# Kernel tuning notes

Measured on AMD Instinct MI355X. Metric: run time of the kernel, lower is better.

The kernel has to match this reference:

```python
import jax, jax.numpy as jnp
import numpy as np


def setup_inputs() -> dict:
    key = jax.random.key(0)
    ks = jax.random.split(key, 7)
    B, T, E, H, V = 32, 200, 32, 128, 8000
    s = lambda fan: 1.0 / np.sqrt(fan)
    return {
        "x": jax.random.normal(ks[0], (B, T, E), dtype=jnp.float32),
        "Ww": jax.random.normal(ks[1], (H, H), dtype=jnp.float32) * s(H),
        "Wb": jax.random.normal(ks[2], (H,), dtype=jnp.float32) * s(H),
        "Uw": jax.random.normal(ks[3], (H, E), dtype=jnp.float32) * s(E),
        "Ub": jax.random.normal(ks[4], (H,), dtype=jnp.float32) * s(E),
        "Vw": jax.random.normal(ks[5], (V, H), dtype=jnp.float32) * s(H),
        "Vb": jax.random.normal(ks[6], (V,), dtype=jnp.float32) * s(H),
    }


def reference(x, Ww, Wb, Uw, Ub, Vw, Vb):
    # x: [B, T, E]. Elman RNN: h_t = tanh(W h_{t-1} + b_W + U x_t + b_U); out_t = V h_t + b_V
    B = x.shape[0]
    H = Ww.shape[0]
    h0 = jnp.zeros((B, H), dtype=x.dtype)
    # Precompute input projections for all timesteps at once: [T, B, H]
    ux = jnp.einsum('bte,he->tbh', x, Uw) + Ub + Wb

    def step(h, ux_t):
        h = jnp.tanh(h @ Ww.T + ux_t)
        return h, h

    hidden, hs = jax.lax.scan(step, h0, ux)  # hs: [T, B, H]
    # Output projection applied to all hidden states (same math as per-step V)
    out_seq = jnp.einsum('tbh,vh->btv', hs, Vw) + Vb  # [B, T, V]
    return out_seq, hidden
```

## Files before the change

### kernel.cpp

```cpp
#include <hip/hip_runtime.h>
#include <stdint.h>

typedef short v8s __attribute__((ext_vector_type(8)));
typedef float v4f __attribute__((ext_vector_type(4)));

__device__ __forceinline__ float bf2f(short s) {
    unsigned int u = ((unsigned int)(unsigned short)s) << 16;
    float f; __builtin_memcpy(&f, &u, 4); return f;
}
__device__ __forceinline__ unsigned short f2bf_rne(float f) {
    unsigned int u; __builtin_memcpy(&u, &f, 4);
    return (unsigned short)((u + 0x7FFFu + ((u >> 16) & 1u)) >> 16);
}
__device__ __forceinline__ unsigned short f2bf_rhu(float f) {
    unsigned int u; __builtin_memcpy(&u, &f, 4);
    return (unsigned short)((u + 0x8000u) >> 16);
}
__device__ __forceinline__ unsigned short f2bf_trunc(float f) {
    unsigned int u; __builtin_memcpy(&u, &f, 4);
    return (unsigned short)(u >> 16);
}
__device__ __forceinline__ float tanh_fast(float z) {
    float e = __expf(2.0f * z);
    float r = __builtin_amdgcn_rcpf(e + 1.0f);
    return __builtin_fmaf(-2.0f, r, 1.0f);
}

__global__ __launch_bounds__(256) void ux_kernel(
    const float* __restrict__ x, const float* __restrict__ Uw,
    const float* __restrict__ Ub, const float* __restrict__ Wb,
    float* __restrict__ ux, unsigned* __restrict__ sync) {
    if (blockIdx.x == 0) {
        for (int i = threadIdx.x; i < 864; i += 256) sync[i] = 0;
    }
    int row = blockIdx.x * 2 + (threadIdx.x >> 7);
    int i = threadIdx.x & 127;
    int b = row & 31, t = row >> 5;
    const float* xr = x + (b * 200 + t) * 32;
    const float* ur = Uw + i * 32;
    float acc = 0.f;
#pragma unroll
    for (int e4 = 0; e4 < 8; ++e4) {
        v4f xv = *(const v4f*)(xr + e4 * 4);
        v4f uv = *(const v4f*)(ur + e4 * 4);
#pragma unroll
        for (int j = 0; j < 4; ++j) acc = __builtin_fmaf(xv[j], uv[j], acc);
    }
    ux[row * 128 + i] = acc + Ub[i] + Wb[i];
}

__global__ __launch_bounds__(512) void fused_kernel(
    const float* __restrict__ Ww, const float* __restrict__ ux,
    short* __restrict__ hs, float* __restrict__ hidden_out,
    const float* __restrict__ Vw, const float* __restrict__ Vb,
    float* __restrict__ out, unsigned* __restrict__ sync) {
    __shared__ alignas(16) short hbuf[2 * 2 * 16 * 136];
    __shared__ unsigned s_ticket;
    const int tid = threadIdx.x;

    if (tid == 0)
        s_ticket = __hip_atomic_fetch_add(sync, 1u, __ATOMIC_RELAXED,
                                          __HIP_MEMORY_SCOPE_AGENT);
    __syncthreads();
    const unsigned ticket = s_ticket;

    const int w = tid >> 6, lane = tid & 63, q = lane >> 4, c = lane & 15;

    if (ticket < 2) {
        char* lds = (char*)hbuf;
        const int b0 = (int)ticket * 16;
        const int col = 16 * w + c;

        for (int i = tid; i < 1088; i += 512)
            ((v8s*)hbuf)[i] = (v8s){0, 0, 0, 0, 0, 0, 0, 0};

        v8s w_hi[4], w_lo[4];
#pragma unroll
        for (int kb = 0; kb < 4; ++kb) {
            const float* p = Ww + col * 128 + 32 * kb + 8 * q;
#pragma unroll
            for (int j = 0; j < 8; ++j) {
                float v = p[j];
                unsigned short hi = f2bf_rne(v);
                w_hi[kb][j] = (short)hi;
                w_lo[kb][j] = (short)f2bf_rne(v - bf2f((short)hi));
            }
        }

        const int rd_base = c * 272 + 16 * q;
        const int wr_base = q * 1088 + col * 2;

        const float* uxp = ux + (b0 + 4 * q) * 128 + col;
        float uxv0 = uxp[0], uxv1 = uxp[128], uxv2 = uxp[256], uxv3 = uxp[384];
        uxp += 4096;
        short* hsp = hs + (b0 + 4 * q) * 128 + col;

        __syncthreads();

#define RNN_STEP(RBUF, WBUF)                                                        \
    {                                                                               \
        float un0 = uxp[0], un1 = uxp[128], un2 = uxp[256], un3 = uxp[384];         \
        v4f a0 = {uxv0, uxv1, uxv2, uxv3};                                          \
        v4f a1 = {0.f, 0.f, 0.f, 0.f}, a2 = a1;                                     \
        _Pragma("unroll") for (int kb = 0; kb < 4; ++kb) {                          \
            v8s ahi = *(const v8s*)(lds + (RBUF)*8704 + kb * 64 + rd_base);         \
            v8s alo = *(const v8s*)(lds + (RBUF)*8704 + 4352 + kb * 64 + rd_base);  \
            a0 = __builtin_amdgcn_mfma_f32_16x16x32_bf16(ahi, w_hi[kb], a0, 0, 0, 0); \
            a1 = __builtin_amdgcn_mfma_f32_16x16x32_bf16(ahi, w_lo[kb], a1, 0, 0, 0); \
            a2 = __builtin_amdgcn_mfma_f32_16x16x32_bf16(alo, w_hi[kb], a2, 0, 0, 0); \
        }                                                                           \
        _Pragma("unroll") for (int r = 0; r < 4; ++r) {                             \
            float z = (a0[r] + a1[r]) + a2[r];                                      \
            float h = tanh_fast(z);                                                 \
            unsigned short hh = f2bf_rhu(h);                                        \
            float rem = h - bf2f((short)hh);                                        \
            unsigned short hl = f2bf_trunc(rem);                                    \
            *(short*)(lds + (WBUF)*8704 + r * 272 + wr_base) = (short)hh;           \
            *(short*)(lds + (WBUF)*8704 + 4352 + r * 272 + wr_base) = (short)hl;    \
            hsp[r * 128] = (short)hh;                                               \
        }                                                                           \
        uxv0 = un0; uxv1 = un1; uxv2 = un2; uxv3 = un3;                             \
        uxp += 4096; hsp += 4096;                                                   \
        __syncthreads();                                                            \
    }

        for (int tp = 0; tp < 100; ++tp) {
            RNN_STEP(0, 1)
            RNN_STEP(1, 0)
            if ((tp & 1) && tid == 0)
                __hip_atomic_fetch_add(sync + 16 + (tp >> 1) * 16, 1u,
                                       __ATOMIC_RELEASE, __HIP_MEMORY_SCOPE_AGENT);
        }
#undef RNN_STEP

#pragma unroll
        for (int r = 0; r < 4; ++r) {
            short hh = *(short*)(lds + r * 272 + wr_base);
            short hl = *(short*)(lds + 4352 + r * 272 + wr_base);
            hidden_out[(b0 + 4 * q + r) * 128 + col] = bf2f(hh) + bf2f(hl);
        }
        return;
    }

    const int cid = (int)ticket - 2;
    const int tb_tile = cid >> 5;
    const int v_tile = cid & 31;
    const int v_wave = v_tile * 256 + 32 * w;
    const int n0 = tb_tile * 128;

    unsigned* flag = sync + 16 + tb_tile * 16;
    if (tid == 0) {
        while (__hip_atomic_load(flag, __ATOMIC_RELAXED,
                                 __HIP_MEMORY_SCOPE_AGENT) < 2u)
            __builtin_amdgcn_s_sleep(32);
        unsigned g = __hip_atomic_load(flag, __ATOMIC_ACQUIRE,
                                       __HIP_MEMORY_SCOPE_AGENT);
        asm volatile("" ::"v"(g));
    }
    __syncthreads();

    v4f acc[2][8];
#pragma unroll
    for (int a = 0; a < 2; ++a)
#pragma unroll
        for (int b = 0; b < 8; ++b) acc[a][b] = (v4f){0.f, 0.f, 0.f, 0.f};

#pragma unroll
    for (int kb = 0; kb < 4; ++kb) {
        v8s afr[2];
#pragma unroll
        for (int vt = 0; vt < 2; ++vt) {
            int vr = v_wave + 16 * vt + c;
            vr = vr < 8000 ? vr : 7999;
            const float* ap = Vw + vr * 128 + 32 * kb + 8 * q;
            v4f p0 = *(const v4f*)ap;
            v4f p1 = *(const v4f*)(ap + 4);
#pragma unroll
            for (int j = 0; j < 4; ++j) {
                afr[vt][j] = (short)f2bf_rne(p0[j]);
                afr[vt][4 + j] = (short)f2bf_rne(p1[j]);
            }
        }
#pragma unroll
        for (int nt = 0; nt < 8; ++nt) {
            v8s bfr = *(const v8s*)(hs + (n0 + 16 * nt + c) * 128 + 32 * kb + 8 * q);
            acc[0][nt] = __builtin_amdgcn_mfma_f32_16x16x32_bf16(afr[0], bfr, acc[0][nt], 0, 0, 0);
            acc[1][nt] = __builtin_amdgcn_mfma_f32_16x16x32_bf16(afr[1], bfr, acc[1][nt], 0, 0, 0);
        }
    }

#pragma unroll
    for (int vt = 0; vt < 2; ++vt) {
        int v4base = v_wave + 16 * vt + 4 * q;
        bool ok = v4base < 8000;
        v4f vbv = *(const v4f*)(Vb + (ok ? v4base : 0));
#pragma unroll
        for (int nt = 0; nt < 8; ++nt) {
            int n = n0 + 16 * nt + c;
            int t = n >> 5, b = n & 31;
            unsigned int off = (unsigned int)(b * 200 + t) * 8000u + (unsigned int)v4base;
            if (ok) {
                v4f o;
#pragma unroll
                for (int r = 0; r < 4; ++r) o[r] = acc[vt][nt][r] + vbv[r];
                *(v4f*)(out + (size_t)off) = o;
            }
        }
    }
}

extern "C" void kernel_launch(void* const* d_in, const int* in_sizes, int n_in,
                              void* d_out, int out_size, void* d_ws, size_t ws_size,
                              hipStream_t stream) {
    const float* x  = (const float*)d_in[0];
    const float* Ww = (const float*)d_in[1];
    const float* Wb = (const float*)d_in[2];
    const float* Uw = (const float*)d_in[3];
    const float* Ub = (const float*)d_in[4];
    const float* Vw = (const float*)d_in[5];
    const float* Vb = (const float*)d_in[6];
    float* out = (float*)d_out;

    float* ux = (float*)d_ws;
    short* hs = (short*)((char*)d_ws + 3276800);
    unsigned* sync = (unsigned*)((char*)d_ws + 4915200);

    ux_kernel<<<3200, 256, 0, stream>>>(x, Uw, Ub, Wb, ux, sync);
    fused_kernel<<<1602, 512, 0, stream>>>(Ww, ux, hs, out + 51200000,
                                           Vw, Vb, out, sync);
}
```

Baseline: 388.2 us.

## Make output-projection blocks persistent and lighten RNN step barriers

The grid shrinks from 1602 to 258 blocks. Each consumer block converts its Vw tile to bf16 once, keeps it in registers, and loops over time tiles with a stride of 256, waiting on each tile's flag. This removes repeated Vw loads and conversions and the cost of launching many blocks. The recurrent blocks now run at raised wave priority and use a raw LDS-wait plus s_barrier on three of every four steps. Progress flags are published every four steps, with 4-step tile granularity kept. The risk is that persistent consumers serialize their tiles and add register pressure from holding afr[4][2].

After: 422.4 us. +8.8%, slower.

```diff
diff --git a/kernel.cpp b/kernel.cpp
--- a/kernel.cpp
+++ b/kernel.cpp
@@ -48,6 +48,8 @@
     }
     ux[row * 128 + i] = acc + Ub[i] + Wb[i];
 }
+
+#define RAWBAR asm volatile("s_waitcnt lgkmcnt(0)\n\ts_barrier" ::: "memory")
 
 __global__ __launch_bounds__(512) void fused_kernel(
     const float* __restrict__ Ww, const float* __restrict__ ux,
@@ -67,6 +69,7 @@
     const int w = tid >> 6, lane = tid & 63, q = lane >> 4, c = lane & 15;
 
     if (ticket < 2) {
+        __builtin_amdgcn_s_setprio(1);
         char* lds = (char*)hbuf;
         const int b0 = (int)ticket * 16;
         const int col = 16 * w + c;
@@ -97,7 +100,7 @@
 
         __syncthreads();
 
-#define RNN_STEP(RBUF, WBUF)                                                        \
+#define RNN_STEP(RBUF, WBUF, SYNC)                                                  \
     {                                                                               \
         float un0 = uxp[0], un1 = uxp[128], un2 = uxp[256], un3 = uxp[384];         \
         v4f a0 = {uxv0, uxv1, uxv2, uxv3};                                          \
@@ -121,14 +124,16 @@
         }                                                                           \
         uxv0 = un0; uxv1 = un1; uxv2 = un2; uxv3 = un3;                             \
         uxp += 4096; hsp += 4096;                                                   \
-        __syncthreads();                                                            \
-    }
-
-        for (int tp = 0; tp < 100; ++tp) {
-            RNN_STEP(0, 1)
-            RNN_STEP(1, 0)
-            if ((tp & 1) && tid == 0)
-                __hip_atomic_fetch_add(sync + 16 + (tp >> 1) * 16, 1u,
+        SYNC;                                                                       \
+    }
+
+        for (int it = 0; it < 50; ++it) {
+            RNN_STEP(0, 1, RAWBAR)
+            RNN_STEP(1, 0, RAWBAR)
+            RNN_STEP(0, 1, RAWBAR)
+            RNN_STEP(1, 0, __syncthreads())
+            if (tid == 0)
+                __hip_atomic_fetch_add(sync + 16 + it * 16, 1u,
                                        __ATOMIC_RELEASE, __HIP_MEMORY_SCOPE_AGENT);
         }
 #undef RNN_STEP
@@ -142,32 +147,13 @@
         return;
     }
 
-    const int cid = (int)ticket - 2;
-    const int tb_tile = cid >> 5;
-    const int v_tile = cid & 31;
+    const int cid0 = (int)ticket - 2;
+    const int v_tile = cid0 & 31;
     const int v_wave = v_tile * 256 + 32 * w;
-    const int n0 = tb_tile * 128;
-
-    unsigned* flag = sync + 16 + tb_tile * 16;
-    if (tid == 0) {
-        while (__hip_atomic_load(flag, __ATOMIC_RELAXED,
-                                 __HIP_MEMORY_SCOPE_AGENT) < 2u)
-            __builtin_amdgcn_s_sleep(32);
-        unsigned g = __hip_atomic_load(flag, __ATOMIC_ACQUIRE,
-                                       __HIP_MEMORY_SCOPE_AGENT);
-        asm volatile("" ::"v"(g));
-    }
-    __syncthreads();
-
-    v4f acc[2][8];
-#pragma unroll
-    for (int a = 0; a < 2; ++a)
-#pragma unroll
-        for (int b = 0; b < 8; ++b) acc[a][b] = (v4f){0.f, 0.f, 0.f, 0.f};
-
-#pragma unroll
-    for (int kb = 0; kb < 4; ++kb) {
-        v8s afr[2];
+
+    v8s afr[4][2];
+#pragma unroll
+    for (int kb = 0; kb < 4; ++kb)
 #pragma unroll
         for (int vt = 0; vt < 2; ++vt) {
             int vr = v_wave + 16 * vt + c;
@@ -177,33 +163,64 @@
             v4f p1 = *(const v4f*)(ap + 4);
 #pragma unroll
             for (int j = 0; j < 4; ++j) {
-                afr[vt][j] = (short)f2bf_rne(p0[j]);
-                afr[vt][4 + j] = (short)f2bf_rne(p1[j]);
-            }
-        }
-#pragma unroll
-        for (int nt = 0; nt < 8; ++nt) {
-            v8s bfr = *(const v8s*)(hs + (n0 + 16 * nt + c) * 128 + 32 * kb + 8 * q);
-            acc[0][nt] = __builtin_amdgcn_mfma_f32_16x16x32_bf16(afr[0], bfr, acc[0][nt], 0, 0, 0);
-            acc[1][nt] = __builtin_amdgcn_mfma_f32_16x16x32_bf16(afr[1], bfr, acc[1][nt], 0, 0, 0);
-        }
-    }
-
+                afr[kb][vt][j] = (short)f2bf_rne(p0[j]);
+                afr[kb][vt][4 + j] = (short)f2bf_rne(p1[j]);
+            }
+        }
+    v4f vbv[2];
+    bool okv[2];
+    int v4b[2];
 #pragma unroll
     for (int vt = 0; vt < 2; ++vt) {
-        int v4base = v_wave + 16 * vt + 4 * q;
-        bool ok = v4base < 8000;
-        v4f vbv = *(const v4f*)(Vb + (ok ? v4base : 0));
-#pragma unroll
-        for (int nt = 0; nt < 8; ++nt) {
-            int n = n0 + 16 * nt + c;
-            int t = n >> 5, b = n & 31;
-            unsigned int off = (unsigned int)(b * 200 + t) * 8000u + (unsigned int)v4base;
-            if (ok) {
-                v4f o;
-#pragma unroll
-                for (int r = 0; r < 4; ++r) o[r] = acc[vt][nt][r] + vbv[r];
-                *(v4f*)(out + (size_t)off) = o;
+        v4b[vt] = v_wave + 16 * vt + 4 * q;
+        okv[vt] = v4b[vt] < 8000;
+        vbv[vt] = *(const v4f*)(Vb + (okv[vt] ? v4b[vt] : 0));
+    }
+
+    for (int cid = cid0; cid < 1600; cid += 256) {
+        const int tb_tile = cid >> 5;
+        const int n0 = tb_tile * 128;
+
+        unsigned* flag = sync + 16 + tb_tile * 16;
+        if (tid == 0) {
+            while (__hip_atomic_load(flag, __ATOMIC_RELAXED,
+                                     __HIP_MEMORY_SCOPE_AGENT) < 2u)
+                __builtin_amdgcn_s_sleep(32);
+            unsigned g = __hip_atomic_load(flag, __ATOMIC_ACQUIRE,
+                                           __HIP_MEMORY_SCOPE_AGENT);
+            asm volatile("" ::"v"(g));
+        }
+        __syncthreads();
+
+        v4f acc[2][8];
+#pragma unroll
+        for (int a = 0; a < 2; ++a)
+#pragma unroll
+            for (int b = 0; b < 8; ++b) acc[a][b] = (v4f){0.f, 0.f, 0.f, 0.f};
+
+#pragma unroll
+        for (int kb = 0; kb < 4; ++kb) {
+#pragma unroll
+            for (int nt = 0; nt < 8; ++nt) {
+                v8s bfr = *(const v8s*)(hs + (n0 + 16 * nt + c) * 128 + 32 * kb + 8 * q);
+                acc[0][nt] = __builtin_amdgcn_mfma_f32_16x16x32_bf16(afr[kb][0], bfr, acc[0][nt], 0, 0, 0);
+                acc[1][nt] = __builtin_amdgcn_mfma_f32_16x16x32_bf16(afr[kb][1], bfr, acc[1][nt], 0, 0, 0);
+            }
+        }
+
+#pragma unroll
+        for (int vt = 0; vt < 2; ++vt) {
+#pragma unroll
+            for (int nt = 0; nt < 8; ++nt) {
+                int n = n0 + 16 * nt + c;
+                int t = n >> 5, b = n & 31;
+                unsigned int off = (unsigned int)(b * 200 + t) * 8000u + (unsigned int)v4b[vt];
+                if (okv[vt]) {
+                    v4f o;
+#pragma unroll
+                    for (int r = 0; r < 4; ++r) o[r] = acc[vt][nt][r] + vbv[vt][r];
+                    *(v4f*)(out + (size_t)off) = o;
+                }
             }
         }
     }
@@ -226,6 +243,6 @@
     unsigned* sync = (unsigned*)((char*)d_ws + 4915200);
 
     ux_kernel<<<3200, 256, 0, stream>>>(x, Uw, Ub, Wb, ux, sync);
-    fused_kernel<<<1602, 512, 0, stream>>>(Ww, ux, hs, out + 51200000,
-                                           Vw, Vb, out, sync);
-}
+    fused_kernel<<<258, 512, 0, stream>>>(Ww, ux, hs, out + 51200000,
+                                          Vw, Vb, out, sync);
+}
```
